# Performance work log

Measured on AMD Instinct MI355X. Metric: run time of the kernel, lower is better.

The kernel has to match this reference:

```python
import jax, jax.numpy as jnp
import numpy as np

NUM_EMBEDDINGS = 2048
EMBEDDING_DIM = 256
COMMITMENT_COST = 0.25


def setup_inputs() -> dict:
    key = jax.random.key(0)
    k1, k2 = jax.random.split(key)
    z_e = jax.random.normal(k1, (65536, EMBEDDING_DIM), dtype=jnp.float32)
    # nn.init.uniform_(weight, -1/K, 1/K)
    emb_w = jax.random.uniform(
        k2, (NUM_EMBEDDINGS, EMBEDDING_DIM), dtype=jnp.float32,
        minval=-1.0 / NUM_EMBEDDINGS, maxval=1.0 / NUM_EMBEDDINGS)
    return {"z_e": z_e, "emb_w": emb_w}


def reference(z_e, emb_w):
    # squared-distance matrix [N, K] = |z|^2 + |e|^2 - 2 z.e
    z_sq = jnp.sum(z_e * z_e, axis=1, keepdims=True)            # [N, 1]
    e_sq = jnp.sum(emb_w * emb_w, axis=1)                       # [K]
    cross = jnp.einsum('nd,kd->nk', z_e, emb_w)                 # [N, K]
    distances = z_sq + e_sq - 2.0 * cross
    encoding_indices = jnp.argmin(distances, axis=1)            # [N] int
    z_q = emb_w[encoding_indices]                               # [N, D]

    codebook_loss = jnp.mean((z_q - jax.lax.stop_gradient(z_e)) ** 2)
    commitment_loss = jnp.mean((z_e - jax.lax.stop_gradient(z_q)) ** 2)
    vq_loss = codebook_loss + COMMITMENT_COST * commitment_loss

    # straight-through estimator
    z_q_st = z_e + jax.lax.stop_gradient(z_q - z_e)
    return (z_q_st, vq_loss, encoding_indices)
```

## Files before the change

kernel.cpp:

```cpp
#include <hip/hip_runtime.h>
#include <cfloat>

#define N_ROWS 65536
#define DIM 256
#define K_CODES 2048
#define MT 128
#define KT 256
#define DC 16
#define BLOCK 256
#define ZSTR (MT + 4)
#define ESTR (KT + 4)
#define NSTAGES ((DIM / DC) * (K_CODES / KT))

typedef float f32x2 __attribute__((ext_vector_type(2)));
typedef float f32x4 __attribute__((ext_vector_type(4)));

#define LOHALF(v) __builtin_shufflevector(v, v, 0, 1)
#define HIHALF(v) __builtin_shufflevector(v, v, 2, 3)

#define PK_FMA_LO(acc, ap, bp) \
    asm("v_pk_fma_f32 %0, %1, %2, %0 op_sel:[0,0,0] op_sel_hi:[0,1,1]" \
        : "+v"(acc) : "v"(ap), "v"(bp))
#define PK_FMA_HI(acc, ap, bp) \
    asm("v_pk_fma_f32 %0, %1, %2, %0 op_sel:[1,0,0] op_sel_hi:[1,1,1]" \
        : "+v"(acc) : "v"(ap), "v"(bp))

__global__ __launch_bounds__(256)
void vq_esq_kernel(const float* __restrict__ emb, float* __restrict__ esq) {
    int w = threadIdx.x >> 6;
    int lane = threadIdx.x & 63;
    int k = blockIdx.x * 4 + w;
    float4 v = *(const float4*)&emb[(size_t)k * DIM + lane * 4];
    float s = v.x * v.x + v.y * v.y + v.z * v.z + v.w * v.w;
    #pragma unroll
    for (int off = 32; off >= 1; off >>= 1) s += __shfl_xor(s, off, 64);
    if (lane == 0) esq[k] = s;
}

__global__ __launch_bounds__(BLOCK, 1)
void vq_main_kernel(const float* __restrict__ z,
                    const float* __restrict__ emb,
                    const float* __restrict__ esq,
                    float* __restrict__ out,
                    float* __restrict__ loss_acc) {
    __shared__ float zS[2][DC][ZSTR];
    __shared__ float eT[2][DC][ESTR];
    __shared__ float zsq_s[MT];
    __shared__ int   best_s[MT];
    __shared__ float lred[4];

    const int tid = threadIdx.x;
    const int m0  = blockIdx.x * MT;
    const int rg  = tid >> 5;
    const int cg  = tid & 31;
    const int esr = tid >> 2;
    const int esf = tid & 3;
    const int zr  = tid >> 1;
    const int zh  = tid & 1;

    {
        const float* zp = &z[(size_t)(m0 + zr) * DIM + zh * 64];
        float sA = 0.f, sB = 0.f;
        #pragma unroll
        for (int d4 = 0; d4 < 16; ++d4) {
            float4 v = *(const float4*)&zp[d4 * 4];
            sA += v.x * v.x; sA += v.y * v.y; sA += v.z * v.z; sA += v.w * v.w;
        }
        #pragma unroll
        for (int d4 = 0; d4 < 16; ++d4) {
            float4 v = *(const float4*)&zp[128 + d4 * 4];
            sB += v.x * v.x; sB += v.y * v.y; sB += v.z * v.z; sB += v.w * v.w;
        }
        float s = sA + sB;
        s += __shfl_down(s, 1, 64);
        if (zh == 0) zsq_s[zr] = s;
    }

    {
        const float* zp = &z[(size_t)(m0 + zr) * DIM + 8 * zh];
        float4 za = *(const float4*)&zp[0];
        float4 zb = *(const float4*)&zp[4];
        zS[0][8 * zh + 0][zr] = za.x;
        zS[0][8 * zh + 1][zr] = za.y;
        zS[0][8 * zh + 2][zr] = za.z;
        zS[0][8 * zh + 3][zr] = za.w;
        zS[0][8 * zh + 4][zr] = zb.x;
        zS[0][8 * zh + 5][zr] = zb.y;
        zS[0][8 * zh + 6][zr] = zb.z;
        zS[0][8 * zh + 7][zr] = zb.w;
        #pragma unroll
        for (int cb = 0; cb < 4; ++cb) {
            int c = esr + cb * 64;
            float4 ev = *(const float4*)&emb[(size_t)c * DIM + 4 * esf];
            eT[0][4 * esf + 0][c] = ev.x;
            eT[0][4 * esf + 1][c] = ev.y;
            eT[0][4 * esf + 2][c] = ev.z;
            eT[0][4 * esf + 3][c] = ev.w;
        }
    }
    __syncthreads();

    float bestv[16];
    int   besti[16];
    #pragma unroll
    for (int j = 0; j < 16; ++j) { bestv[j] = FLT_MAX; besti[j] = 0; }

    f32x2 acc2[16][4];

    for (int s = 0; s < NSTAGES; ++s) {
        const int p     = s & 1;
        const int kt    = (s >> 4) * KT;
        const int dcIdx = s & 15;

        if (dcIdx == 0) {
            #pragma unroll
            for (int j = 0; j < 16; ++j)
                #pragma unroll
                for (int i2 = 0; i2 < 4; ++i2) acc2[j][i2] = (f32x2){0.f, 0.f};
        }

        const int sn  = (s + 1 < NSTAGES) ? s + 1 : s;
        const int nkt = (sn >> 4) * KT;
        const int ndc = (sn & 15) * DC;
        float4 zn0 = *(const float4*)&z[(size_t)(m0 + zr) * DIM + ndc + 8 * zh];
        float4 zn1 = *(const float4*)&z[(size_t)(m0 + zr) * DIM + ndc + 8 * zh + 4];
        float4 en0 = *(const float4*)&emb[(size_t)(nkt + esr +   0) * DIM + ndc + 4 * esf];
        float4 en1 = *(const float4*)&emb[(size_t)(nkt + esr +  64) * DIM + ndc + 4 * esf];
        float4 en2 = *(const float4*)&emb[(size_t)(nkt + esr + 128) * DIM + ndc + 4 * esf];
        float4 en3 = *(const float4*)&emb[(size_t)(nkt + esr + 192) * DIM + ndc + 4 * esf];

        #pragma unroll
        for (int d = 0; d < DC; ++d) {
            f32x4 a0 = *(const f32x4*)&zS[p][d][16 * rg];
            f32x4 a1 = *(const f32x4*)&zS[p][d][16 * rg + 4];
            f32x4 a2 = *(const f32x4*)&zS[p][d][16 * rg + 8];
            f32x4 a3 = *(const f32x4*)&zS[p][d][16 * rg + 12];
            f32x4 b0 = *(const f32x4*)&eT[p][d][4 * cg];
            f32x4 b1 = *(const f32x4*)&eT[p][d][128 + 4 * cg];
            f32x2 ap[8] = { LOHALF(a0), HIHALF(a0), LOHALF(a1), HIHALF(a1),
                            LOHALF(a2), HIHALF(a2), LOHALF(a3), HIHALF(a3) };
            f32x2 bp[4] = { LOHALF(b0), HIHALF(b0), LOHALF(b1), HIHALF(b1) };
            #pragma unroll
            for (int jp = 0; jp < 8; ++jp) {
                #pragma unroll
                for (int i2 = 0; i2 < 4; ++i2) {
                    PK_FMA_LO(acc2[2 * jp][i2],     ap[jp], bp[i2]);
                    PK_FMA_HI(acc2[2 * jp + 1][i2], ap[jp], bp[i2]);
                }
            }
        }

        {
            const int q = p ^ 1;
            zS[q][8 * zh + 0][zr] = zn0.x;
            zS[q][8 * zh + 1][zr] = zn0.y;
            zS[q][8 * zh + 2][zr] = zn0.z;
            zS[q][8 * zh + 3][zr] = zn0.w;
            zS[q][8 * zh + 4][zr] = zn1.x;
            zS[q][8 * zh + 5][zr] = zn1.y;
            zS[q][8 * zh + 6][zr] = zn1.z;
            zS[q][8 * zh + 7][zr] = zn1.w;
            eT[q][4 * esf + 0][esr      ] = en0.x;
            eT[q][4 * esf + 1][esr      ] = en0.y;
            eT[q][4 * esf + 2][esr      ] = en0.z;
            eT[q][4 * esf + 3][esr      ] = en0.w;
            eT[q][4 * esf + 0][esr +  64] = en1.x;
            eT[q][4 * esf + 1][esr +  64] = en1.y;
            eT[q][4 * esf + 2][esr +  64] = en1.z;
            eT[q][4 * esf + 3][esr +  64] = en1.w;
            eT[q][4 * esf + 0][esr + 128] = en2.x;
            eT[q][4 * esf + 1][esr + 128] = en2.y;
            eT[q][4 * esf + 2][esr + 128] = en2.z;
            eT[q][4 * esf + 3][esr + 128] = en2.w;
            eT[q][4 * esf + 0][esr + 192] = en3.x;
            eT[q][4 * esf + 1][esr + 192] = en3.y;
            eT[q][4 * esf + 2][esr + 192] = en3.z;
            eT[q][4 * esf + 3][esr + 192] = en3.w;
        }

        if (dcIdx == 15) {
            float4 e0 = *(const float4*)&esq[kt + 4 * cg];
            float4 e1 = *(const float4*)&esq[kt + 128 + 4 * cg];
            float es[8] = {e0.x, e0.y, e0.z, e0.w, e1.x, e1.y, e1.z, e1.w};
            #pragma unroll
            for (int j = 0; j < 16; ++j) {
                float zs = zsq_s[16 * rg + j];
                #pragma unroll
                for (int i = 0; i < 8; ++i) {
                    float aij  = acc2[j][i >> 1][i & 1];
                    float t    = zs + es[i];
                    float dist = t - 2.0f * aij;
                    int idx = (i < 4) ? (kt + 4 * cg + i) : (kt + 128 + 4 * cg + (i - 4));
                    bool better = (dist < bestv[j]);
                    bestv[j] = better ? dist : bestv[j];
                    besti[j] = better ? idx  : besti[j];
                }
            }
        }
        __syncthreads();
    }

    #pragma unroll
    for (int off = 16; off >= 1; off >>= 1) {
        #pragma unroll
        for (int j = 0; j < 16; ++j) {
            float ov = __shfl_xor(bestv[j], off, 64);
            int   oi = __shfl_xor(besti[j], off, 64);
            bool take = (ov < bestv[j]) || (ov == bestv[j] && oi < besti[j]);
            bestv[j] = take ? ov : bestv[j];
            besti[j] = take ? oi : besti[j];
        }
    }
    if (cg == 0) {
        #pragma unroll
        for (int j = 0; j < 16; ++j) best_s[16 * rg + j] = besti[j];
    }
    __syncthreads();

    float lsum = 0.f;
    const int d4 = tid & 63;
    for (int it = 0; it < 32; ++it) {
        int r  = (tid >> 6) + it * 4;
        int bk = best_s[r];
        float4 q4 = *(const float4*)&emb[(size_t)bk * DIM + 4 * d4];
        float4 z4 = *(const float4*)&z[(size_t)(m0 + r) * DIM + 4 * d4];
        float4 o;
        float dx;
        dx = q4.x - z4.x; o.x = z4.x + dx; lsum = fmaf(dx, dx, lsum);
        dx = q4.y - z4.y; o.y = z4.y + dx; lsum = fmaf(dx, dx, lsum);
        dx = q4.z - z4.z; o.z = z4.z + dx; lsum = fmaf(dx, dx, lsum);
        dx = q4.w - z4.w; o.w = z4.w + dx; lsum = fmaf(dx, dx, lsum);
        *(float4*)&out[(size_t)(m0 + r) * DIM + 4 * d4] = o;
    }
    #pragma unroll
    for (int off = 32; off >= 1; off >>= 1) lsum += __shfl_xor(lsum, off, 64);
    if ((tid & 63) == 0) lred[tid >> 6] = lsum;
    __syncthreads();
    if (tid == 0) {
        float bs = lred[0] + lred[1] + lred[2] + lred[3];
        atomicAdd(loss_acc, bs);
    }
    if (tid < MT) out[(size_t)N_ROWS * DIM + 1 + m0 + tid] = (float)best_s[tid];
}

__global__ void vq_finalize_kernel(const float* __restrict__ loss_acc,
                                   float* __restrict__ out) {
    double s = (double)loss_acc[0];
    out[(size_t)N_ROWS * DIM] = (float)(s * 1.25 / ((double)N_ROWS * (double)DIM));
}

extern "C" void kernel_launch(void* const* d_in, const int* in_sizes, int n_in,
                              void* d_out, int out_size, void* d_ws, size_t ws_size,
                              hipStream_t stream) {
    (void)in_sizes; (void)n_in; (void)out_size; (void)ws_size;
    const float* z   = (const float*)d_in[0];
    const float* emb = (const float*)d_in[1];
    float* out = (float*)d_out;
    float* ws  = (float*)d_ws;
    float* loss_acc = ws;
    float* esq      = ws + 64;

    hipMemsetAsync(d_ws, 0, sizeof(float), stream);
    vq_esq_kernel<<<K_CODES / 4, 256, 0, stream>>>(emb, esq);
    vq_main_kernel<<<N_ROWS / MT, BLOCK, 0, stream>>>(z, emb, esq, out, loss_acc);
    vq_finalize_kernel<<<1, 1, 0, stream>>>(loss_acc, out);
}
```

Baseline: 833.7 us.

## Use split-bf16 MFMA GEMM with top-2 candidates and fp32 rescue pass

Replaces the fp32 packed-FMA distance GEMM with a bf16 MFMA GEMM that splits z and the codebook into three bf16 pieces (hi/mid/lo) and accumulates six cross products to approximate fp32 accuracy. Each row keeps its top-2 candidates per column-half, and a rescue kernel recomputes the exact fp32 distance for the four candidates, picks the argmin, and writes outputs and loss. It adds split-conversion passes, about 100MB of workspace traffic and extra launches. The old path remains as a fallback when the workspace is too small.

Measured after the change: 2.778 ms. 3.33x slower.

```diff
diff --git a/kernel.cpp b/kernel.cpp
--- a/kernel.cpp
+++ b/kernel.cpp
@@ -4,6 +4,265 @@
 #define N_ROWS 65536
 #define DIM 256
 #define K_CODES 2048
+
+typedef float f32x2 __attribute__((ext_vector_type(2)));
+typedef float f32x4 __attribute__((ext_vector_type(4)));
+typedef short short8 __attribute__((ext_vector_type(8)));
+
+__device__ __forceinline__ unsigned short f2bf(float x) {
+    unsigned u = __float_as_uint(x);
+    u += 0x7fffu + ((u >> 16) & 1u);
+    return (unsigned short)(u >> 16);
+}
+__device__ __forceinline__ float bf2f(unsigned short b) {
+    return __uint_as_float(((unsigned)b) << 16);
+}
+
+#define GLL16(gp, lp) \
+    __builtin_amdgcn_global_load_lds((const __attribute__((address_space(1))) void*)(gp), \
+                                     (__attribute__((address_space(3))) void*)(lp), 16, 0, 0)
+
+__global__ __launch_bounds__(256)
+void vq_esq_kernel(const float* __restrict__ emb, float* __restrict__ esq) {
+    int w = threadIdx.x >> 6;
+    int lane = threadIdx.x & 63;
+    int k = blockIdx.x * 4 + w;
+    float4 v = *(const float4*)&emb[(size_t)k * DIM + lane * 4];
+    float s = v.x * v.x + v.y * v.y + v.z * v.z + v.w * v.w;
+    #pragma unroll
+    for (int off = 32; off >= 1; off >>= 1) s += __shfl_xor(s, off, 64);
+    if (lane == 0) esq[k] = s;
+}
+
+__global__ __launch_bounds__(256)
+void vq_zsq_kernel(const float* __restrict__ z, float* __restrict__ zsq_g) {
+    const int tid = threadIdx.x;
+    const int m0 = blockIdx.x * 128;
+    const int zr = tid >> 1, zh = tid & 1;
+    const float* zp = &z[(size_t)(m0 + zr) * DIM + zh * 64];
+    float sA = 0.f, sB = 0.f;
+    #pragma unroll
+    for (int d4 = 0; d4 < 16; ++d4) {
+        float4 v = *(const float4*)&zp[d4 * 4];
+        sA += v.x * v.x; sA += v.y * v.y; sA += v.z * v.z; sA += v.w * v.w;
+    }
+    #pragma unroll
+    for (int d4 = 0; d4 < 16; ++d4) {
+        float4 v = *(const float4*)&zp[128 + d4 * 4];
+        sB += v.x * v.x; sB += v.y * v.y; sB += v.z * v.z; sB += v.w * v.w;
+    }
+    float s = sA + sB;
+    s += __shfl_down(s, 1, 64);
+    if (zh == 0) zsq_g[m0 + zr] = s;
+}
+
+__global__ __launch_bounds__(256)
+void vq_split_kernel(const float* __restrict__ src,
+                     unsigned short* __restrict__ H,
+                     unsigned short* __restrict__ M,
+                     unsigned short* __restrict__ L) {
+    const size_t i = (size_t)blockIdx.x * 256 + threadIdx.x;
+    float4 v = *(const float4*)&src[4 * i];
+    ushort4 h, m, l;
+    #define SPLIT1(c) { \
+        h.c = f2bf(v.c); float hf = bf2f(h.c); float r = v.c - hf;    \
+        m.c = f2bf(r);   float mf_ = bf2f(m.c); float r2 = r - mf_;   \
+        l.c = f2bf(r2);   }
+    SPLIT1(x) SPLIT1(y) SPLIT1(z) SPLIT1(w)
+    #undef SPLIT1
+    *(ushort4*)&H[4 * i] = h;
+    *(ushort4*)&M[4 * i] = m;
+    *(ushort4*)&L[4 * i] = l;
+}
+
+__global__ __launch_bounds__(256, 1)
+void vq_gemm_kernel(const unsigned short* __restrict__ Zh,
+                    const unsigned short* __restrict__ Zm,
+                    const unsigned short* __restrict__ Zl,
+                    const unsigned short* __restrict__ Eh,
+                    const unsigned short* __restrict__ Em,
+                    const unsigned short* __restrict__ El,
+                    const float* __restrict__ zsq_g,
+                    const float* __restrict__ esq_g,
+                    int* __restrict__ top2) {
+    __shared__ unsigned short ldsA[2][128 * 32];
+    __shared__ unsigned short ldsB[2][128 * 32];
+    __shared__ float zsq_s[128];
+
+    const int tid  = threadIdx.x;
+    const int m0   = blockIdx.x * 128;
+    const int wid  = tid >> 6;
+    const int lane = tid & 63;
+    const int wm   = wid >> 1;
+    const int wn   = wid & 1;
+    const int srow = lane >> 2;
+    const int schkG = (lane & 3) ^ (srow & 3);
+
+    if (tid < 128) zsq_s[tid] = zsq_g[m0 + tid];
+
+    float b1v[16], b2v[16];
+    int   b1i[16], b2i[16];
+    #pragma unroll
+    for (int r = 0; r < 16; ++r) {
+        b1v[r] = FLT_MAX; b2v[r] = FLT_MAX;
+        b1i[r] = 0x7fffffff; b2i[r] = 0x7fffffff;
+    }
+
+    auto stage = [&](int nt, int kk, int b) {
+        const int s  = kk >> 3;
+        const int d0 = (kk & 7) * 32;
+        const unsigned short* Ap = (s == 4) ? Zl : ((s == 2 || s == 5) ? Zm : Zh);
+        const unsigned short* Bp = (s == 3) ? El : ((s == 1 || s == 5) ? Em : Eh);
+        #pragma unroll
+        for (int i = 0; i < 2; ++i) {
+            const int rr = wid * 32 + i * 16;
+            const unsigned short* ga = Ap + (size_t)(m0 + rr + srow) * DIM + d0 + schkG * 8;
+            GLL16(ga, &ldsA[b][rr * 32]);
+            const unsigned short* gb = Bp + (size_t)(nt * 128 + rr + srow) * DIM + d0 + schkG * 8;
+            GLL16(gb, &ldsB[b][rr * 32]);
+        }
+    };
+
+    stage(0, 0, 0);
+    __syncthreads();
+
+    int p = 0;
+    for (int nt = 0; nt < 16; ++nt) {
+        f32x4 acc[4][4];
+        #pragma unroll
+        for (int a = 0; a < 4; ++a)
+            #pragma unroll
+            for (int bb = 0; bb < 4; ++bb)
+                acc[a][bb] = (f32x4){0.f, 0.f, 0.f, 0.f};
+
+        #pragma unroll 1
+        for (int kk = 0; kk < 48; ++kk) {
+            int kn = kk + 1, ntn = nt;
+            if (kn == 48) { kn = 0; ntn = nt + 1; if (ntn == 16) { ntn = 15; kn = 47; } }
+            stage(ntn, kn, p ^ 1);
+
+            const int kc = lane >> 4;
+            short8 aF[4], bF[4];
+            #pragma unroll
+            for (int mf = 0; mf < 4; ++mf) {
+                const int row = wm * 64 + mf * 16 + (lane & 15);
+                aF[mf] = *(const short8*)((const char*)&ldsA[p][0] + row * 64 + ((kc ^ (row & 3)) << 4));
+            }
+            #pragma unroll
+            for (int nf = 0; nf < 4; ++nf) {
+                const int row = wn * 64 + nf * 16 + (lane & 15);
+                bF[nf] = *(const short8*)((const char*)&ldsB[p][0] + row * 64 + ((kc ^ (row & 3)) << 4));
+            }
+            #pragma unroll
+            for (int mf = 0; mf < 4; ++mf)
+                #pragma unroll
+                for (int nf = 0; nf < 4; ++nf)
+                    acc[mf][nf] = __builtin_amdgcn_mfma_f32_16x16x32_bf16(aF[mf], bF[nf], acc[mf][nf], 0, 0, 0);
+
+            __syncthreads();
+            p ^= 1;
+        }
+
+        float zsv[16];
+        #pragma unroll
+        for (int mf = 0; mf < 4; ++mf)
+            #pragma unroll
+            for (int rg = 0; rg < 4; ++rg)
+                zsv[mf * 4 + rg] = zsq_s[wm * 64 + mf * 16 + (lane >> 4) * 4 + rg];
+        #pragma unroll
+        for (int nf = 0; nf < 4; ++nf) {
+            const int code = nt * 128 + wn * 64 + nf * 16 + (lane & 15);
+            const float es = esq_g[code];
+            #pragma unroll
+            for (int mf = 0; mf < 4; ++mf) {
+                #pragma unroll
+                for (int rg = 0; rg < 4; ++rg) {
+                    const int r = mf * 4 + rg;
+                    float t = zsv[r] + es;
+                    float dist = t - 2.0f * acc[mf][nf][rg];
+                    bool better1 = (dist < b1v[r]) || (dist == b1v[r] && code < b1i[r]);
+                    float ob1v = b1v[r]; int ob1i = b1i[r];
+                    if (better1) { b1v[r] = dist; b1i[r] = code; }
+                    float dv = better1 ? ob1v : dist;
+                    int   di = better1 ? ob1i : code;
+                    bool ins2 = (dv < b2v[r]) || (dv == b2v[r] && di < b2i[r]);
+                    if (ins2) { b2v[r] = dv; b2i[r] = di; }
+                }
+            }
+        }
+    }
+
+    #pragma unroll
+    for (int r = 0; r < 16; ++r) {
+        #pragma unroll
+        for (int off = 1; off <= 8; off <<= 1) {
+            float o1v = __shfl_xor(b1v[r], off, 64); int o1i = __shfl_xor(b1i[r], off, 64);
+            float o2v = __shfl_xor(b2v[r], off, 64); int o2i = __shfl_xor(b2i[r], off, 64);
+            bool t1 = (o1v < b1v[r]) || (o1v == b1v[r] && o1i < b1i[r]);
+            float dv = t1 ? b1v[r] : o1v; int di = t1 ? b1i[r] : o1i;
+            if (t1) { b1v[r] = o1v; b1i[r] = o1i; }
+            bool t2 = (dv < b2v[r]) || (dv == b2v[r] && di < b2i[r]);
+            if (t2) { b2v[r] = dv; b2i[r] = di; }
+            bool t3 = (o2v < b2v[r]) || (o2v == b2v[r] && o2i < b2i[r]);
+            if (t3) { b2v[r] = o2v; b2i[r] = o2i; }
+        }
+    }
+    if ((lane & 15) == 0) {
+        #pragma unroll
+        for (int r = 0; r < 16; ++r) {
+            const int rowg = m0 + wm * 64 + (r >> 2) * 16 + (lane >> 4) * 4 + (r & 3);
+            top2[rowg * 4 + wn * 2 + 0] = b1i[r];
+            top2[rowg * 4 + wn * 2 + 1] = b2i[r];
+        }
+    }
+}
+
+__global__ __launch_bounds__(256)
+void vq_rescue_kernel(const float* __restrict__ z, const float* __restrict__ emb,
+                      const float* __restrict__ zsq_g, const float* __restrict__ esq_g,
+                      const int* __restrict__ top2,
+                      float* __restrict__ out, float* __restrict__ loss_acc) {
+    __shared__ float lred[4];
+    const int tid = threadIdx.x;
+    const int wid = tid >> 6, lane = tid & 63;
+    const int row = blockIdx.x * 4 + wid;
+    const int cand = top2[row * 4 + (lane & 3)];
+    const float* zr = z + (size_t)row * DIM;
+    const float* er = emb + (size_t)cand * DIM;
+    float a = 0.f;
+    #pragma unroll 8
+    for (int d4 = 0; d4 < 64; ++d4) {
+        float4 zv = *(const float4*)&zr[4 * d4];
+        float4 ev = *(const float4*)&er[4 * d4];
+        a = fmaf(zv.x, ev.x, a); a = fmaf(zv.y, ev.y, a);
+        a = fmaf(zv.z, ev.z, a); a = fmaf(zv.w, ev.w, a);
+    }
+    float t = zsq_g[row] + esq_g[cand];
+    float dist = t - 2.0f * a;
+    int best = cand;
+    #pragma unroll
+    for (int off = 1; off <= 2; off <<= 1) {
+        float ov = __shfl_xor(dist, off, 64);
+        int   oi = __shfl_xor(best, off, 64);
+        bool tk = (ov < dist) || (ov == dist && oi < best);
+        dist = tk ? ov : dist; best = tk ? oi : best;
+    }
+    float4 q4 = *(const float4*)&emb[(size_t)best * DIM + 4 * lane];
+    float4 z4 = *(const float4*)&zr[4 * lane];
+    float4 o; float dx, lsum = 0.f;
+    dx = q4.x - z4.x; o.x = z4.x + dx; lsum = fmaf(dx, dx, lsum);
+    dx = q4.y - z4.y; o.y = z4.y + dx; lsum = fmaf(dx, dx, lsum);
+    dx = q4.z - z4.z; o.z = z4.z + dx; lsum = fmaf(dx, dx, lsum);
+    dx = q4.w - z4.w; o.w = z4.w + dx; lsum = fmaf(dx, dx, lsum);
+    *(float4*)&out[(size_t)row * DIM + 4 * lane] = o;
+    #pragma unroll
+    for (int off = 32; off >= 1; off >>= 1) lsum += __shfl_xor(lsum, off, 64);
+    if (lane == 0) lred[wid] = lsum;
+    __syncthreads();
+    if (tid == 0) atomicAdd(loss_acc, lred[0] + lred[1] + lred[2] + lred[3]);
+    if (lane == 0) out[(size_t)N_ROWS * DIM + 1 + row] = (float)best;
+}
+
 #define MT 128
 #define KT 256
 #define DC 16
@@ -12,30 +271,14 @@
 #define ESTR (KT + 4)
 #define NSTAGES ((DIM / DC) * (K_CODES / KT))
 
-typedef float f32x2 __attribute__((ext_vector_type(2)));
-typedef float f32x4 __attribute__((ext_vector_type(4)));
-
 #define LOHALF(v) __builtin_shufflevector(v, v, 0, 1)
 #define HIHALF(v) __builtin_shufflevector(v, v, 2, 3)
-
 #define PK_FMA_LO(acc, ap, bp) \
     asm("v_pk_fma_f32 %0, %1, %2, %0 op_sel:[0,0,0] op_sel_hi:[0,1,1]" \
         : "+v"(acc) : "v"(ap), "v"(bp))
 #define PK_FMA_HI(acc, ap, bp) \
     asm("v_pk_fma_f32 %0, %1, %2, %0 op_sel:[1,0,0] op_sel_hi:[1,1,1]" \
         : "+v"(acc) : "v"(ap), "v"(bp))
-
-__global__ __launch_bounds__(256)
-void vq_esq_kernel(const float* __restrict__ emb, float* __restrict__ esq) {
-    int w = threadIdx.x >> 6;
-    int lane = threadIdx.x & 63;
-    int k = blockIdx.x * 4 + w;
-    float4 v = *(const float4*)&emb[(size_t)k * DIM + lane * 4];
-    float s = v.x * v.x + v.y * v.y + v.z * v.z + v.w * v.w;
-    #pragma unroll
-    for (int off = 32; off >= 1; off >>= 1) s += __shfl_xor(s, off, 64);
-    if (lane == 0) esq[k] = s;
-}
 
 __global__ __launch_bounds__(BLOCK, 1)
 void vq_main_kernel(const float* __restrict__ z,
@@ -75,27 +318,20 @@
         s += __shfl_down(s, 1, 64);
         if (zh == 0) zsq_s[zr] = s;
     }
-
     {
         const float* zp = &z[(size_t)(m0 + zr) * DIM + 8 * zh];
         float4 za = *(const float4*)&zp[0];
         float4 zb = *(const float4*)&zp[4];
-        zS[0][8 * zh + 0][zr] = za.x;
-        zS[0][8 * zh + 1][zr] = za.y;
-        zS[0][8 * zh + 2][zr] = za.z;
-        zS[0][8 * zh + 3][zr] = za.w;
-        zS[0][8 * zh + 4][zr] = zb.x;
-        zS[0][8 * zh + 5][zr] = zb.y;
-        zS[0][8 * zh + 6][zr] = zb.z;
-        zS[0][8 * zh + 7][zr] = zb.w;
+        zS[0][8 * zh + 0][zr] = za.x; zS[0][8 * zh + 1][zr] = za.y;
+        zS[0][8 * zh + 2][zr] = za.z; zS[0][8 * zh + 3][zr] = za.w;
+        zS[0][8 * zh + 4][zr] = zb.x; zS[0][8 * zh + 5][zr] = zb.y;
+        zS[0][8 * zh + 6][zr] = zb.z; zS[0][8 * zh + 7][zr] = zb.w;
         #pragma unroll
         for (int cb = 0; cb < 4; ++cb) {
             int c = esr + cb * 64;
             float4 ev = *(const float4*)&emb[(size_t)c * DIM + 4 * esf];
-            eT[0][4 * esf + 0][c] = ev.x;
-            eT[0][4 * esf + 1][c] = ev.y;
-            eT[0][4 * esf + 2][c] = ev.z;
-            eT[0][4 * esf + 3][c] = ev.w;
+            eT[0][4 * esf + 0][c] = ev.x; eT[0][4 * esf + 1][c] = ev.y;
+            eT[0][4 * esf + 2][c] = ev.z; eT[0][4 * esf + 3][c] = ev.w;
         }
     }
     __syncthreads();
@@ -149,35 +385,21 @@
                 }
             }
         }
-
         {
             const int q = p ^ 1;
-            zS[q][8 * zh + 0][zr] = zn0.x;
-            zS[q][8 * zh + 1][zr] = zn0.y;
-            zS[q][8 * zh + 2][zr] = zn0.z;
-            zS[q][8 * zh + 3][zr] = zn0.w;
-            zS[q][8 * zh + 4][zr] = zn1.x;
-            zS[q][8 * zh + 5][zr] = zn1.y;
-            zS[q][8 * zh + 6][zr] = zn1.z;
-            zS[q][8 * zh + 7][zr] = zn1.w;
-            eT[q][4 * esf + 0][esr      ] = en0.x;
-            eT[q][4 * esf + 1][esr      ] = en0.y;
-            eT[q][4 * esf + 2][esr      ] = en0.z;
-            eT[q][4 * esf + 3][esr      ] = en0.w;
-            eT[q][4 * esf + 0][esr +  64] = en1.x;
-            eT[q][4 * esf + 1][esr +  64] = en1.y;
-            eT[q][4 * esf + 2][esr +  64] = en1.z;
-            eT[q][4 * esf + 3][esr +  64] = en1.w;
-            eT[q][4 * esf + 0][esr + 128] = en2.x;
-            eT[q][4 * esf + 1][esr + 128] = en2.y;
-            eT[q][4 * esf + 2][esr + 128] = en2.z;
-            eT[q][4 * esf + 3][esr + 128] = en2.w;
-            eT[q][4 * esf + 0][esr + 192] = en3.x;
-            eT[q][4 * esf + 1][esr + 192] = en3.y;
-            eT[q][4 * esf + 2][esr + 192] = en3.z;
-            eT[q][4 * esf + 3][esr + 192] = en3.w;
-        }
-
+            zS[q][8 * zh + 0][zr] = zn0.x; zS[q][8 * zh + 1][zr] = zn0.y;
+            zS[q][8 * zh + 2][zr] = zn0.z; zS[q][8 * zh + 3][zr] = zn0.w;
+            zS[q][8 * zh + 4][zr] = zn1.x; zS[q][8 * zh + 5][zr] = zn1.y;
+            zS[q][8 * zh + 6][zr] = zn1.z; zS[q][8 * zh + 7][zr] = zn1.w;
+            eT[q][4 * esf + 0][esr      ] = en0.x; eT[q][4 * esf + 1][esr      ] = en0.y;
+            eT[q][4 * esf + 2][esr      ] = en0.z; eT[q][4 * esf + 3][esr      ] = en0.w;
+            eT[q][4 * esf + 0][esr +  64] = en1.x; eT[q][4 * esf + 1][esr +  64] = en1.y;
+            eT[q][4 * esf + 2][esr +  64] = en1.z; eT[q][4 * esf + 3][esr +  64] = en1.w;
+            eT[q][4 * esf + 0][esr + 128] = en2.x; eT[q][4 * esf + 1][esr + 128] = en2.y;
+            eT[q][4 * esf + 2][esr + 128] = en2.z; eT[q][4 * esf + 3][esr + 128] = en2.w;
+            eT[q][4 * esf + 0][esr + 192] = en3.x; eT[q][4 * esf + 1][esr + 192] = en3.y;
+            eT[q][4 * esf + 2][esr + 192] = en3.z; eT[q][4 * esf + 3][esr + 192] = en3.w;
+        }
         if (dcIdx == 15) {
             float4 e0 = *(const float4*)&esq[kt + 4 * cg];
             float4 e1 = *(const float4*)&esq[kt + 128 + 4 * cg];
@@ -252,16 +474,36 @@
 extern "C" void kernel_launch(void* const* d_in, const int* in_sizes, int n_in,
                               void* d_out, int out_size, void* d_ws, size_t ws_size,
                               hipStream_t stream) {
-    (void)in_sizes; (void)n_in; (void)out_size; (void)ws_size;
+    (void)in_sizes; (void)n_in; (void)out_size;
     const float* z   = (const float*)d_in[0];
     const float* emb = (const float*)d_in[1];
     float* out = (float*)d_out;
-    float* ws  = (float*)d_ws;
-    float* loss_acc = ws;
-    float* esq      = ws + 64;
+    char* wsb = (char*)d_ws;
+    float* loss_acc = (float*)wsb;
+    float* esq      = (float*)(wsb + 1024);
 
     hipMemsetAsync(d_ws, 0, sizeof(float), stream);
     vq_esq_kernel<<<K_CODES / 4, 256, 0, stream>>>(emb, esq);
-    vq_main_kernel<<<N_ROWS / MT, BLOCK, 0, stream>>>(z, emb, esq, out, loss_acc);
+
+    const size_t NEED = (size_t)104 << 20;
+    if (ws_size >= NEED) {
+        float* zsq_g = (float*)(wsb + 16384);
+        int*   top2  = (int*)(wsb + ((size_t)1 << 19));
+        unsigned short* Eh = (unsigned short*)(wsb + ((size_t)2 << 20));
+        unsigned short* Em = (unsigned short*)(wsb + ((size_t)3 << 20));
+        unsigned short* El = (unsigned short*)(wsb + ((size_t)4 << 20));
+        unsigned short* Zh = (unsigned short*)(wsb + ((size_t)8 << 20));
+        unsigned short* Zm = (unsigned short*)(wsb + ((size_t)40 << 20));
+        unsigned short* Zl = (unsigned short*)(wsb + ((size_t)72 << 20));
+        vq_zsq_kernel<<<N_ROWS / 128, 256, 0, stream>>>(z, zsq_g);
+        vq_split_kernel<<<(N_ROWS * DIM) / 1024, 256, 0, stream>>>(z, Zh, Zm, Zl);
+        vq_split_kernel<<<(K_CODES * DIM) / 1024, 256, 0, stream>>>(emb, Eh, Em, El);
+        vq_gemm_kernel<<<N_ROWS / 128, 256, 0, stream>>>(Zh, Zm, Zl, Eh, Em, El,
+                                                         zsq_g, esq, top2);
+        vq_rescue_kernel<<<N_ROWS / 4, 256, 0, stream>>>(z, emb, zsq_g, esq, top2,
+                                                         out, loss_acc);
+    } else {
+        vq_main_kernel<<<N_ROWS / MT, BLOCK, 0, stream>>>(z, emb, esq, out, loss_acc);
+    }
     vq_finalize_kernel<<<1, 1, 0, stream>>>(loss_acc, out);
 }
```
